# Performance work log

Measured on AMD Instinct MI355X. Metric: run time of the kernel, lower is better.

## Reference

```python
import jax, jax.numpy as jnp
import numpy as np

IN_CH = 4          # qubits
KSZ = 3            # kernel size
NUM_KERNELS = 2
LAYERS = 1
STRIDE = 1
DILATION = 1
NPOS = KSZ * KSZ
TOTAL_W = NPOS * LAYERS * IN_CH * 3  # 108


def setup_inputs() -> dict:
    key = jax.random.key(0)
    k1, k2 = jax.random.split(key)
    x = jax.random.normal(k1, (16, IN_CH, 64, 64), dtype=jnp.float32)
    weights = jax.random.uniform(k2, (NUM_KERNELS, TOTAL_W), minval=-np.pi, maxval=np.pi, dtype=jnp.float32)
    return {"x": x, "weights": weights}


def _apply_1q(state, U, q):
    # state: (N, 2,...,2) with IN_CH qubit axes; U: (2,2) shared or (N,2,2) batched
    s = jnp.moveaxis(state, q + 1, -1)
    if U.ndim == 2:
        s = jnp.einsum('ab,...b->...a', U, s)
    else:
        s = jnp.einsum('nab,n...b->n...a', U, s)
    return jnp.moveaxis(s, -1, q + 1)


def _ry_mat(theta):
    c = jnp.cos(theta / 2)
    s = jnp.sin(theta / 2)
    return jnp.stack([jnp.stack([c, -s], -1), jnp.stack([s, c], -1)], -2).astype(jnp.complex64)


def _rx_mat(theta):
    c = jnp.cos(theta / 2).astype(jnp.complex64)
    s = (-1j) * jnp.sin(theta / 2).astype(jnp.complex64)
    return jnp.stack([jnp.stack([c, s], -1), jnp.stack([s, c], -1)], -2)


def _rz_mat(theta):
    e = jnp.exp((-0.5j) * theta.astype(jnp.complex64))
    z = jnp.zeros_like(e)
    return jnp.stack([jnp.stack([e, z], -1), jnp.stack([z, jnp.conj(e)], -1)], -2)


def _cx(state, cq, tq):
    s = jnp.moveaxis(state, (cq + 1, tq + 1), (-2, -1))
    s = s.at[..., 1, :].set(s[..., 1, ::-1])  # flip target where control=1
    return jnp.moveaxis(s, (-2, -1), (cq + 1, tq + 1))


def _circuit(w_flat, patches):
    # patches: (N, IN_CH, NPOS) data angles; w_flat: (TOTAL_W,)
    n = IN_CH
    N = patches.shape[0]
    dim = 2 ** n
    # H on every qubit from |0...0> == uniform superposition with + amplitudes
    state = jnp.full((N,) + (2,) * n, 1.0 / np.sqrt(dim), dtype=jnp.complex64)
    w = w_flat.reshape(NPOS, LAYERS, n, 3)
    for pos in range(NPOS):
        for ch in range(n):
            state = _apply_1q(state, _ry_mat(patches[:, ch, pos]), ch)
        for l in range(LAYERS):
            for q in range(n):
                state = _apply_1q(state, _rx_mat(w[pos, l, q, 0]), q)
                state = _apply_1q(state, _ry_mat(w[pos, l, q, 1]), q)
                state = _apply_1q(state, _rz_mat(w[pos, l, q, 2]), q)
            for q in range(n - 1):
                state = _cx(state, q, q + 1)
            if n > 1:
                state = _cx(state, n - 1, 0)
    p = jnp.abs(state) ** 2  # (N, 2,...,2)
    sign = jnp.array([1.0, -1.0], dtype=jnp.float32)
    exps = []
    for q in range(n):
        sh = [1] * (n + 1)
        sh[q + 1] = 2
        exps.append(jnp.sum(p * sign.reshape(sh), axis=tuple(range(1, n + 1))))
    return jnp.stack(exps, -1)  # (N, n) <Z_q> expectations


def _extract_patches(x):
    B, C, H, W = x.shape
    out_h = (H - (KSZ - 1) * DILATION - 1) // STRIDE + 1
    out_w = (W - (KSZ - 1) * DILATION - 1) // STRIDE + 1
    hh = (jnp.arange(out_h) * STRIDE)[:, None] + jnp.arange(KSZ)[None, :] * DILATION  # (out_h, K)
    ww = (jnp.arange(out_w) * STRIDE)[:, None] + jnp.arange(KSZ)[None, :] * DILATION  # (out_w, K)
    p = x[:, :, hh][:, :, :, :, ww]                  # (B, C, out_h, K, out_w, K)
    p = p.transpose(0, 2, 4, 1, 3, 5)                # (B, out_h, out_w, C, K, K)
    return p.reshape(B, out_h * out_w, C, KSZ * KSZ), out_h, out_w


def reference(x, weights):
    B, C, H, W = x.shape
    patches, out_h, out_w = _extract_patches(x)
    flat = patches.reshape(B * out_h * out_w, C, KSZ * KSZ)
    outs = []
    for kidx in range(NUM_KERNELS):
        e = _circuit(weights[kidx], flat)                       # (B*P, C)
        e = e.reshape(B, out_h, out_w, C).transpose(0, 3, 1, 2)  # (B, C, out_h, out_w)
        outs.append(e)
    return jnp.concatenate(outs, axis=1)  # (B, NUM_KERNELS*C, out_h, out_w)
```

## Files before the change

### kernel.cpp

```cpp
#include <hip/hip_runtime.h>
#include <math.h>

#define IN_CH 4
#define KSZ 3
#define NUM_KERNELS 2
#define NPOS 9
#define HH 64
#define WW 64
#define BB 16
#define OH 62
#define OW 62
#define NPATCH (BB*OH*OW)
#define NU (NPOS*IN_CH)
#define CHST (HH*WW)
#define BLK 64
#define UF4 (NUM_KERNELS*NU*4)

__global__ void qk_precompute(const float* __restrict__ w, float* __restrict__ U) {
    int t = blockIdx.x * blockDim.x + threadIdx.x;
    if (t >= NUM_KERNELS * NU) return;
    int k   = t / NU;
    int rem = t % NU;
    const float* wp = w + k * (NU * 3) + rem * 3;
    float hx = 0.5f * wp[0], hy = 0.5f * wp[1], hz = 0.5f * wp[2];
    float cx = cosf(hx), sx = sinf(hx);
    float cy = cosf(hy), sy = sinf(hy);
    float cz = cosf(hz), sz = sinf(hz);
    float m00r =  cy * cx, m00i =  sy * sx;
    float m01r = -sy * cx, m01i = -cy * sx;
    float* o = U + t * 4;
    o[0] = cz * m00r + sz * m00i;  o[1] = cz * m00i - sz * m00r;
    o[2] = cz * m01r + sz * m01i;  o[3] = cz * m01i - sz * m01r;
}

__device__ __forceinline__ void gate2(float sr[16], float si[16], const int mask,
                                      const float far_, const float fai,
                                      const float fbr, const float fbi) {
    #pragma unroll
    for (int i = 0; i < 16; ++i) {
        if (i & mask) continue;
        const int j = i | mask;
        float ar = sr[i], ai = si[i], br = sr[j], bi = si[j];
        sr[i] =  far_ * ar - fai * ai + fbr * br - fbi * bi;
        si[i] =  far_ * ai + fai * ar + fbr * bi + fbi * br;
        sr[j] = -fbr * ar - fbi * ai + far_ * br + fai * bi;
        si[j] =  fbi * ar - fbr * ai - fai * br + far_ * bi;
    }
}

__device__ __forceinline__ void cx_ring(float sr[16], float si[16]) {
    #pragma unroll
    for (int e = 0; e < 4; ++e) {
        const int cmask = 8 >> e;
        const int tmask = 8 >> ((e + 1) & 3);
        #pragma unroll
        for (int i = 0; i < 16; ++i) {
            if ((i & cmask) && !(i & tmask)) {
                const int j = i | tmask;
                float tr = sr[i]; sr[i] = sr[j]; sr[j] = tr;
                float ti = si[i]; si[i] = si[j]; si[j] = ti;
            }
        }
    }
}

__global__ __launch_bounds__(BLK) void qk_main(const float* __restrict__ x,
                                               const float* __restrict__ Uglob,
                                               float* __restrict__ out) {
    __shared__ float sU[UF4];
    const int tid = threadIdx.x;
    for (int t = tid; t < UF4; t += BLK) sU[t] = Uglob[t];
    __syncthreads();

    const int p   = blockIdx.x * BLK + tid;
    const int b   = p / (OH * OW);
    const int rem = p - b * (OH * OW);
    const int oh  = rem / OW;
    const int ow  = rem - oh * OW;
    const float* xp = x + b * (IN_CH * CHST) + oh * WW + ow;

    float s0r[16], s0i[16], s1r[16], s1i[16];
    #pragma unroll
    for (int i = 0; i < 16; ++i) {
        s0r[i] = 0.25f; s0i[i] = 0.0f;
        s1r[i] = 0.25f; s1i[i] = 0.0f;
    }

    #pragma unroll
    for (int kh = 0; kh < KSZ; ++kh) {
        #pragma unroll
        for (int kw = 0; kw < KSZ; ++kw) {
            const int pos = kh * KSZ + kw;
            #pragma unroll
            for (int q = 0; q < IN_CH; ++q) {
                const float th = xp[q * CHST + kh * WW + kw];
                float s, c;
                __sincosf(0.5f * th, &s, &c);
                const int mask = 8 >> q;
                {
                    const float* u = &sU[(pos * IN_CH + q) * 4];
                    const float far_ = c * u[0] + s * u[2], fai = c * u[1] + s * u[3];
                    const float fbr  = c * u[2] - s * u[0], fbi = c * u[3] - s * u[1];
                    gate2(s0r, s0i, mask, far_, fai, fbr, fbi);
                }
                {
                    const float* u = &sU[(NU + pos * IN_CH + q) * 4];
                    const float far_ = c * u[0] + s * u[2], fai = c * u[1] + s * u[3];
                    const float fbr  = c * u[2] - s * u[0], fbi = c * u[3] - s * u[1];
                    gate2(s1r, s1i, mask, far_, fai, fbr, fbi);
                }
            }
            cx_ring(s0r, s0i);
            cx_ring(s1r, s1i);
        }
    }

    float p20[16], p21[16];
    #pragma unroll
    for (int i = 0; i < 16; ++i) {
        p20[i] = s0r[i] * s0r[i] + s0i[i] * s0i[i];
        p21[i] = s1r[i] * s1r[i] + s1i[i] * s1i[i];
    }

    float* ob = out + ((size_t)(b * (NUM_KERNELS * IN_CH)) * OH + oh) * OW + ow;
    #pragma unroll
    for (int q = 0; q < IN_CH; ++q) {
        const int mask = 8 >> q;
        float e0 = 0.0f, e1 = 0.0f;
        #pragma unroll
        for (int i = 0; i < 16; ++i) {
            e0 += (i & mask) ? -p20[i] : p20[i];
            e1 += (i & mask) ? -p21[i] : p21[i];
        }
        ob[(size_t)q * (OH * OW)]            = e0;
        ob[(size_t)(IN_CH + q) * (OH * OW)]  = e1;
    }
}

extern "C" void kernel_launch(void* const* d_in, const int* in_sizes, int n_in,
                              void* d_out, int out_size, void* d_ws, size_t ws_size,
                              hipStream_t stream) {
    const float* x = (const float*)d_in[0];
    const float* w = (const float*)d_in[1];
    float* out = (float*)d_out;
    float* U   = (float*)d_ws;

    hipLaunchKernelGGL(qk_precompute, dim3(1), dim3(128), 0, stream, w, U);
    hipLaunchKernelGGL(qk_main, dim3(NPATCH / BLK), dim3(BLK), 0, stream, x, U, out);
}
```

Before: 78.80 us.

## Split statevector across lane pairs with DPP swaps and kernel index on grid

```diff
diff --git a/kernel.cpp b/kernel.cpp
--- a/kernel.cpp
+++ b/kernel.cpp
@@ -14,7 +14,7 @@
 #define NU (NPOS*IN_CH)
 #define CHST (HH*WW)
 #define BLK 64
-#define UF4 (NUM_KERNELS*NU*4)
+#define UF4K (NU*4)
 
 __global__ void qk_precompute(const float* __restrict__ w, float* __restrict__ U) {
     int t = blockIdx.x * blockDim.x + threadIdx.x;
@@ -33,108 +33,149 @@
     o[2] = cz * m01r + sz * m01i;  o[3] = cz * m01i - sz * m01r;
 }
 
-__device__ __forceinline__ void gate2(float sr[16], float si[16], const int mask,
-                                      const float far_, const float fai,
-                                      const float fbr, const float fbi) {
-    #pragma unroll
-    for (int i = 0; i < 16; ++i) {
-        if (i & mask) continue;
-        const int j = i | mask;
-        float ar = sr[i], ai = si[i], br = sr[j], bi = si[j];
-        sr[i] =  far_ * ar - fai * ai + fbr * br - fbi * bi;
-        si[i] =  far_ * ai + fai * ar + fbr * bi + fbi * br;
-        sr[j] = -fbr * ar - fbi * ai + far_ * br + fai * bi;
-        si[j] =  fbi * ar - fbr * ai - fai * br + far_ * bi;
-    }
+__device__ __forceinline__ float pswap(float v) {
+    return __int_as_float(__builtin_amdgcn_mov_dpp(__float_as_int(v), 0xB1, 0xF, 0xF, true));
 }
 
-__device__ __forceinline__ void cx_ring(float sr[16], float si[16]) {
+template<int MASK>
+__device__ __forceinline__ void gate_local(float Lr[8], float Li[8],
+                                           float far_, float fai,
+                                           float fbr, float fbi) {
     #pragma unroll
-    for (int e = 0; e < 4; ++e) {
-        const int cmask = 8 >> e;
-        const int tmask = 8 >> ((e + 1) & 3);
-        #pragma unroll
-        for (int i = 0; i < 16; ++i) {
-            if ((i & cmask) && !(i & tmask)) {
-                const int j = i | tmask;
-                float tr = sr[i]; sr[i] = sr[j]; sr[j] = tr;
-                float ti = si[i]; si[i] = si[j]; si[j] = ti;
-            }
-        }
+    for (int i = 0; i < 8; ++i) {
+        if (i & MASK) continue;
+        const int j = i | MASK;
+        float ar = Lr[i], ai = Li[i], br = Lr[j], bi = Li[j];
+        Lr[i] =  far_ * ar - fai * ai + fbr * br - fbi * bi;
+        Li[i] =  far_ * ai + fai * ar + fbr * bi + fbi * br;
+        Lr[j] = -fbr * ar - fbi * ai + far_ * br + fai * bi;
+        Li[j] =  fbi * ar - fbr * ai - fai * br + far_ * bi;
     }
 }
 
 __global__ __launch_bounds__(BLK) void qk_main(const float* __restrict__ x,
                                                const float* __restrict__ Uglob,
                                                float* __restrict__ out) {
-    __shared__ float sU[UF4];
-    const int tid = threadIdx.x;
-    for (int t = tid; t < UF4; t += BLK) sU[t] = Uglob[t];
+    __shared__ float sU[UF4K];
+    const int kidx = blockIdx.y;
+    const int tid  = threadIdx.x;
+    for (int t = tid; t < UF4K; t += BLK) sU[t] = Uglob[kidx * UF4K + t];
     __syncthreads();
 
-    const int p   = blockIdx.x * BLK + tid;
+    const int hi   = tid & 1;
+    const float sgnf = hi ? -1.0f : 1.0f;
+    const int p   = blockIdx.x * (BLK / 2) + (tid >> 1);
     const int b   = p / (OH * OW);
     const int rem = p - b * (OH * OW);
     const int oh  = rem / OW;
     const int ow  = rem - oh * OW;
     const float* xp = x + b * (IN_CH * CHST) + oh * WW + ow;
 
-    float s0r[16], s0i[16], s1r[16], s1i[16];
+    float Lr[8], Li[8];
     #pragma unroll
-    for (int i = 0; i < 16; ++i) {
-        s0r[i] = 0.25f; s0i[i] = 0.0f;
-        s1r[i] = 0.25f; s1i[i] = 0.0f;
-    }
+    for (int i = 0; i < 8; ++i) { Lr[i] = 0.25f; Li[i] = 0.0f; }
 
     #pragma unroll
     for (int kh = 0; kh < KSZ; ++kh) {
         #pragma unroll
         for (int kw = 0; kw < KSZ; ++kw) {
             const int pos = kh * KSZ + kw;
-            #pragma unroll
-            for (int q = 0; q < IN_CH; ++q) {
-                const float th = xp[q * CHST + kh * WW + kw];
+            const float* xq = xp + kh * WW + kw;
+
+            {
                 float s, c;
-                __sincosf(0.5f * th, &s, &c);
-                const int mask = 8 >> q;
-                {
-                    const float* u = &sU[(pos * IN_CH + q) * 4];
-                    const float far_ = c * u[0] + s * u[2], fai = c * u[1] + s * u[3];
-                    const float fbr  = c * u[2] - s * u[0], fbi = c * u[3] - s * u[1];
-                    gate2(s0r, s0i, mask, far_, fai, fbr, fbi);
-                }
-                {
-                    const float* u = &sU[(NU + pos * IN_CH + q) * 4];
-                    const float far_ = c * u[0] + s * u[2], fai = c * u[1] + s * u[3];
-                    const float fbr  = c * u[2] - s * u[0], fbi = c * u[3] - s * u[1];
-                    gate2(s1r, s1i, mask, far_, fai, fbr, fbi);
+                __sincosf(0.5f * xq[0], &s, &c);
+                const float* u = &sU[(pos * IN_CH + 0) * 4];
+                const float far_ = c * u[0] + s * u[2], fai = c * u[1] + s * u[3];
+                const float fbr  = c * u[2] - s * u[0], fbi = c * u[3] - s * u[1];
+                const float o0r = far_,        o0i = sgnf * fai;
+                const float o1r = sgnf * fbr,  o1i = fbi;
+                float orr[8], ori[8];
+                #pragma unroll
+                for (int i = 0; i < 8; ++i) { orr[i] = pswap(Lr[i]); ori[i] = pswap(Li[i]); }
+                #pragma unroll
+                for (int i = 0; i < 8; ++i) {
+                    float ar = Lr[i], ai = Li[i], br = orr[i], bi = ori[i];
+                    Lr[i] = o0r * ar - o0i * ai + o1r * br - o1i * bi;
+                    Li[i] = o0r * ai + o0i * ar + o1r * bi + o1i * br;
                 }
             }
-            cx_ring(s0r, s0i);
-            cx_ring(s1r, s1i);
+            {
+                float s, c;
+                __sincosf(0.5f * xq[1 * CHST], &s, &c);
+                const float* u = &sU[(pos * IN_CH + 1) * 4];
+                gate_local<4>(Lr, Li, c * u[0] + s * u[2], c * u[1] + s * u[3],
+                                      c * u[2] - s * u[0], c * u[3] - s * u[1]);
+            }
+            {
+                float s, c;
+                __sincosf(0.5f * xq[2 * CHST], &s, &c);
+                const float* u = &sU[(pos * IN_CH + 2) * 4];
+                gate_local<2>(Lr, Li, c * u[0] + s * u[2], c * u[1] + s * u[3],
+                                      c * u[2] - s * u[0], c * u[3] - s * u[1]);
+            }
+            {
+                float s, c;
+                __sincosf(0.5f * xq[3 * CHST], &s, &c);
+                const float* u = &sU[(pos * IN_CH + 3) * 4];
+                gate_local<1>(Lr, Li, c * u[0] + s * u[2], c * u[1] + s * u[3],
+                                      c * u[2] - s * u[0], c * u[3] - s * u[1]);
+            }
+
+            #pragma unroll
+            for (int i = 0; i < 4; ++i) {
+                const int j = i + 4;
+                float ar = Lr[i], ai = Li[i], br = Lr[j], bi = Li[j];
+                Lr[i] = hi ? br : ar;  Li[i] = hi ? bi : ai;
+                Lr[j] = hi ? ar : br;  Li[j] = hi ? ai : bi;
+            }
+            #pragma unroll
+            for (int i = 0; i < 8; ++i) {
+                if ((i & 4) && !(i & 2)) {
+                    const int j = i | 2;
+                    float tr = Lr[i]; Lr[i] = Lr[j]; Lr[j] = tr;
+                    float ti = Li[i]; Li[i] = Li[j]; Li[j] = ti;
+                }
+            }
+            #pragma unroll
+            for (int i = 0; i < 8; ++i) {
+                if ((i & 2) && !(i & 1)) {
+                    const int j = i | 1;
+                    float tr = Lr[i]; Lr[i] = Lr[j]; Lr[j] = tr;
+                    float ti = Li[i]; Li[i] = Li[j]; Li[j] = ti;
+                }
+            }
+            #pragma unroll
+            for (int i = 1; i < 8; i += 2) {
+                Lr[i] = pswap(Lr[i]);
+                Li[i] = pswap(Li[i]);
+            }
         }
     }
 
-    float p20[16], p21[16];
+    float p2[8];
     #pragma unroll
-    for (int i = 0; i < 16; ++i) {
-        p20[i] = s0r[i] * s0r[i] + s0i[i] * s0i[i];
-        p21[i] = s1r[i] * s1r[i] + s1i[i] * s1i[i];
+    for (int i = 0; i < 8; ++i) p2[i] = Lr[i] * Lr[i] + Li[i] * Li[i];
+
+    float e[4];
+    {
+        float t0 = 0.f, t1 = 0.f, t2 = 0.f, t3 = 0.f;
+        #pragma unroll
+        for (int i = 0; i < 8; ++i) {
+            t0 += p2[i];
+            t1 += (i & 4) ? -p2[i] : p2[i];
+            t2 += (i & 2) ? -p2[i] : p2[i];
+            t3 += (i & 1) ? -p2[i] : p2[i];
+        }
+        e[0] = sgnf * t0; e[1] = t1; e[2] = t2; e[3] = t3;
     }
+    #pragma unroll
+    for (int q = 0; q < 4; ++q) e[q] += pswap(e[q]);
 
-    float* ob = out + ((size_t)(b * (NUM_KERNELS * IN_CH)) * OH + oh) * OW + ow;
-    #pragma unroll
-    for (int q = 0; q < IN_CH; ++q) {
-        const int mask = 8 >> q;
-        float e0 = 0.0f, e1 = 0.0f;
-        #pragma unroll
-        for (int i = 0; i < 16; ++i) {
-            e0 += (i & mask) ? -p20[i] : p20[i];
-            e1 += (i & mask) ? -p21[i] : p21[i];
-        }
-        ob[(size_t)q * (OH * OW)]            = e0;
-        ob[(size_t)(IN_CH + q) * (OH * OW)]  = e1;
-    }
+    float* ob = out + ((size_t)(b * (NUM_KERNELS * IN_CH) + kidx * IN_CH) * OH + oh) * OW + ow;
+    const int qb = hi * 2;
+    ob[(size_t)(qb + 0) * (OH * OW)] = e[qb + 0];
+    ob[(size_t)(qb + 1) * (OH * OW)] = e[qb + 1];
 }
 
 extern "C" void kernel_launch(void* const* d_in, const int* in_sizes, int n_in,
@@ -146,5 +187,6 @@
     float* U   = (float*)d_ws;
 
     hipLaunchKernelGGL(qk_precompute, dim3(1), dim3(128), 0, stream, w, U);
-    hipLaunchKernelGGL(qk_main, dim3(NPATCH / BLK), dim3(BLK), 0, stream, x, U, out);
+    dim3 grid(NPATCH / (BLK / 2), NUM_KERNELS);
+    hipLaunchKernelGGL(qk_main, grid, dim3(BLK), 0, stream, x, U, out);
 }
```

Measured after the change: 88.97 us. 1.13x slower.
